# Kernel tuning notes

Measured on AMD Instinct MI355X. Metric: run time of the kernel, lower is better.

Reference implementation:

```python
import jax, jax.numpy as jnp
import numpy as np
import math

H = 128          # node_dim == hidden_dim
TED = 128        # time_emb_dim
T = 64
BN = 4096


def _mlp(x, w1, b1, w2, b2):
    # 2-layer MLP with SiLU, matching MLP(n_layer=2, act_fn=SiLU)
    return jax.nn.silu(x @ w1 + b1) @ w2 + b2


def _timestep_embedding(t, dim):
    # get_timestep_embedding for possibly-negative relative indices
    half = dim // 2
    freqs = jnp.exp(jnp.arange(half, dtype=jnp.float32) * (-math.log(10000.0) / (half - 1)))
    arg = t.astype(jnp.float32)[:, None] * freqs[None, :]
    return jnp.concatenate([jnp.sin(arg), jnp.cos(arg)], axis=-1)


def setup_inputs() -> dict:
    key = jax.random.key(0)
    ks = jax.random.split(key, 20)
    s = 1.0 / math.sqrt(H)
    d = {
        "x": jax.random.normal(ks[0], (BN, 3, T), jnp.float32),
        "h": jax.random.normal(ks[1], (BN, H, T), jnp.float32),
        "q_w1": jax.random.normal(ks[2], (H, H), jnp.float32) * s,
        "q_b1": jnp.zeros((H,), jnp.float32),
        "q_w2": jax.random.normal(ks[3], (H, H), jnp.float32) * s,
        "q_b2": jnp.zeros((H,), jnp.float32),
        "k_w1": jax.random.normal(ks[4], (H, H), jnp.float32) * s,
        "k_b1": jnp.zeros((H,), jnp.float32),
        "k_w2": jax.random.normal(ks[5], (H, H), jnp.float32) * s,
        "k_b2": jnp.zeros((H,), jnp.float32),
        "v_w1": jax.random.normal(ks[6], (H, H), jnp.float32) * s,
        "v_b1": jnp.zeros((H,), jnp.float32),
        "v_w2": jax.random.normal(ks[7], (H, H), jnp.float32) * s,
        "v_b2": jnp.zeros((H,), jnp.float32),
        "xm_w1": jax.random.normal(ks[8], (H, H), jnp.float32) * s,
        "xm_b1": jnp.zeros((H,), jnp.float32),
        "xm_w2": jax.random.normal(ks[9], (H, 1), jnp.float32) * s,
        "xm_b2": jnp.zeros((1,), jnp.float32),
        "t_w": jax.random.normal(ks[10], (TED, H), jnp.float32) * (1.0 / math.sqrt(TED)),
        "t_b": jnp.zeros((H,), jnp.float32),
    }
    return d


def reference(x, h, q_w1, q_b1, q_w2, q_b2, k_w1, k_b1, k_w2, k_b2,
              v_w1, v_b1, v_w2, v_b2, xm_w1, xm_b1, xm_w2, xm_b2, t_w, t_b):
    Tn = x.shape[-1]
    # relative time embedding E[t, s, :] of shape [T, T, H]
    ti = jnp.arange(Tn)
    rel = (ti[:, None] - ti[None, :]).reshape(-1)
    E = (_timestep_embedding(rel, TED) @ t_w + t_b).reshape(Tn, Tn, -1)

    # merge_time_dim: [N, H, T] -> [N*T, H]  (token order: node-major, time-minor)
    tok = h.transpose(0, 2, 1)                      # [N, T, H]
    q = _mlp(tok, q_w1, q_b1, q_w2, q_b2)           # [N, T, H]
    k = _mlp(tok, k_w1, k_b1, k_w2, k_b2)           # [N, T, H]
    v = _mlp(tok, v_w1, v_b1, v_w2, v_b2)           # [N, T, H]
    vx = _mlp(v, xm_w1, xm_b1, xm_w2, xm_b2)[..., 0]  # [N, T]

    # scores: q . (k_s + E_ts)  -- decomposed, avoids materializing k_ts [N,H,T,T]
    scores = jnp.einsum('nth,nsh->nts', q, k) + jnp.einsum('nth,tsh->nts', q, E)
    alpha = jax.nn.softmax(scores, axis=-1)          # [N, T, S]

    # h update: sum_s alpha * (v_s + E_ts)
    dh = jnp.einsum('nts,nsh->nth', alpha, v) + jnp.einsum('nts,tsh->nth', alpha, E)
    h_out = h + dh.transpose(0, 2, 1)                # [N, H, T]

    # x update: x_t += sum_s alpha[t,s] * vx[s] * (x_t - x_s)
    w = alpha * vx[:, None, :]                       # [N, T, S]
    x_out = x + x * jnp.sum(w, axis=-1)[:, None, :] - jnp.einsum('nts,nds->ndt', w, x)
    return (x_out, h_out)
```

## Files before the change

kernel.cpp:

```cpp
#include <hip/hip_runtime.h>
#include <hip/hip_bf16.h>
#include <math.h>

#define NN 4096

typedef __attribute__((ext_vector_type(8))) short s8v;
typedef __attribute__((ext_vector_type(4))) float f4v;
typedef __attribute__((ext_vector_type(4))) unsigned int u32x4;
typedef __attribute__((ext_vector_type(2))) unsigned int u32x2;
typedef unsigned short u16;

static __device__ __forceinline__ f4v MFMA16(s8v a, s8v b, f4v c) {
  return __builtin_amdgcn_mfma_f32_16x16x32_bf16(a, b, c, 0, 0, 0);
}
static __device__ __forceinline__ u16 f2bf(float f) {
  union { float f; unsigned int u; } v; v.f = f;
  unsigned int r = v.u + 0x7fffu + ((v.u >> 16) & 1u);
  return (u16)(r >> 16);
}
static __device__ __forceinline__ float bf2f(u16 u) {
  union { unsigned int u; float f; } v; v.u = ((unsigned int)u) << 16;
  return v.f;
}
static __device__ __forceinline__ unsigned int cvt2u(float lo, float hi) {
  __hip_bfloat162 h = __float22bfloat162_rn(make_float2(lo, hi));
  union { __hip_bfloat162 b; unsigned int u; } c; c.b = h; return c.u;
}
static __device__ __forceinline__ float silu(float v) {
  return v * __builtin_amdgcn_rcpf(1.0f + __expf(-v));
}

#define SW(row, byte)  ((row) * 256 + ((byte) ^ (((row) & 7) << 4)))

#define FA_OFF 0
#define FB_OFF 49152
#define FC_OFF 98304
#define FD_OFF 131072

__global__ void prep_kernel(const float* __restrict__ qw1, const float* __restrict__ kw1,
                            const float* __restrict__ vw1, const float* __restrict__ qw2,
                            const float* __restrict__ kw2, const float* __restrict__ vw2,
                            const float* __restrict__ xmw1,
                            const float* __restrict__ t_w, const float* __restrict__ t_b,
                            u16* __restrict__ wsb) {
  const int b = blockIdx.x, tid = threadIdx.x;
  const int kt = tid >> 6, l = tid & 63, lr = l & 15, lk = l >> 4;
  if (b < 56) {
    const float* W; int mt; u16* base;
    if (b < 24)      { base = wsb + FA_OFF; mt = b;      W = (b < 8) ? qw1 : (b < 16) ? kw1 : vw1; }
    else if (b < 48) { base = wsb + FB_OFF; mt = b - 24; W = (mt < 8) ? qw2 : (mt < 16) ? kw2 : vw2; }
    else             { base = wsb + FC_OFF; mt = b - 48; W = xmw1; }
    const int ch = (mt & 7) * 16;
    u16 o[8];
#pragma unroll
    for (int j = 0; j < 8; ++j) o[j] = f2bf(W[(kt * 32 + lk * 8 + j) * 128 + ch + lr]);
    u32x4 pk;
#pragma unroll
    for (int i = 0; i < 4; ++i) pk[i] = (unsigned int)o[2 * i] | ((unsigned int)o[2 * i + 1] << 16);
    *(u32x4*)&base[((mt * 4 + kt) * 64 + l) * 8] = pk;
  } else {
    const int rt = b - 56;
    const int r = rt * 16 + lr;
    const float rel = (float)(r - 63);
    const int h0 = kt * 32 + lk * 8;
    float acc[8];
#pragma unroll
    for (int j = 0; j < 8; ++j) acc[j] = t_b[h0 + j];
    const float C = -logf(10000.0f) / 63.0f;
    for (int i = 0; i < 64; ++i) {
      float f = expf((float)i * C);
      float a = rel * f;
      float sn = sinf(a), cs = cosf(a);
#pragma unroll
      for (int j = 0; j < 8; ++j) acc[j] = fmaf(sn, t_w[i * 128 + h0 + j], acc[j]);
#pragma unroll
      for (int j = 0; j < 8; ++j) acc[j] = fmaf(cs, t_w[(i + 64) * 128 + h0 + j], acc[j]);
    }
    u16 o[8];
#pragma unroll
    for (int j = 0; j < 8; ++j) o[j] = f2bf(acc[j]);
    u32x4 pk;
#pragma unroll
    for (int i = 0; i < 4; ++i) pk[i] = (unsigned int)o[2 * i] | ((unsigned int)o[2 * i + 1] << 16);
    *(u32x4*)&wsb[FC_OFF + (((8 + rt) * 4 + kt) * 64 + l) * 8] = pk;
    const int ct = h0 >> 4, lrp = h0 & 15;
    const int ktp = r >> 5, lkp = (r >> 3) & 3, jp = r & 7;
#pragma unroll
    for (int j = 0; j < 8; ++j)
      wsb[FD_OFF + ((ct * 4 + ktp) * 64 + lkp * 16 + lrp + j) * 8 + jp] = o[j];
  }
}

static __device__ __forceinline__ void ldfrag(s8v* dst, const u16* __restrict__ base,
                                              int tile, int l) {
#pragma unroll
  for (int kt = 0; kt < 4; ++kt) dst[kt] = *(const s8v*)&base[tile * 2048 + kt * 512 + l * 8];
}

template <bool SILU, bool HASB>
static __device__ __forceinline__ void gemm2(const s8v* f0, const s8v* f1,
                                             const unsigned char* Bl, unsigned char* Ol,
                                             const float* __restrict__ bias, int mt0,
                                             int lr, int lk, int swm, const int* rb) {
  f4v acc[2][4];
#pragma unroll
  for (int mi = 0; mi < 2; ++mi) {
    float bj[4];
#pragma unroll
    for (int j = 0; j < 4; ++j) bj[j] = HASB ? bias[(mt0 + mi) * 16 + lk * 4 + j] : 0.f;
#pragma unroll
    for (int ni = 0; ni < 4; ++ni)
#pragma unroll
      for (int j = 0; j < 4; ++j) acc[mi][ni][j] = bj[j];
  }
  __builtin_amdgcn_s_setprio(1);
#pragma unroll
  for (int kt = 0; kt < 4; ++kt) {
    s8v a0 = f0[kt], a1 = f1[kt];
#pragma unroll
    for (int ni = 0; ni < 4; ++ni) {
      s8v b = *(const s8v*)(Bl + ni * 4096 + rb[kt]);
      acc[0][ni] = MFMA16(a0, b, acc[0][ni]);
      acc[1][ni] = MFMA16(a1, b, acc[1][ni]);
    }
  }
  __builtin_amdgcn_s_setprio(0);
#pragma unroll
  for (int mi = 0; mi < 2; ++mi) {
    const int ob = lr * 256 + ((((mt0 + mi) * 32) + lk * 8) ^ swm);
#pragma unroll
    for (int ni = 0; ni < 4; ++ni) {
      float v0 = acc[mi][ni][0], v1 = acc[mi][ni][1], v2 = acc[mi][ni][2], v3 = acc[mi][ni][3];
      if (SILU) { v0 = silu(v0); v1 = silu(v1); v2 = silu(v2); v3 = silu(v3); }
      u32x2 st; st[0] = cvt2u(v0, v1); st[1] = cvt2u(v2, v3);
      *(u32x2*)(Ol + ni * 4096 + ob) = st;
    }
  }
}

__launch_bounds__(512, 4)
__global__ void et_main(const float* __restrict__ xg, const float* __restrict__ hg,
                        const u16* __restrict__ wsb,
                        const float* __restrict__ qb1, const float* __restrict__ qb2,
                        const float* __restrict__ kb1,
                        const float* __restrict__ vb1, const float* __restrict__ vb2,
                        const float* __restrict__ xmb1, const float* __restrict__ xmw2,
                        const float* __restrict__ xmb2,
                        float* __restrict__ xout, float* __restrict__ hout) {
  __shared__ __align__(16) unsigned char smem[81920];
  unsigned char* S0 = smem;
  unsigned char* S1 = smem + 16384;
  unsigned char* S2 = smem + 32768;
  unsigned char* S3 = smem + 49152;
  unsigned char* S4 = smem + 65536;
  unsigned char* ALP = S2;
  unsigned char* YB  = S2 + 8192;
  float* XLS = (float*)(S2 + 10240);
  float* VXP = (float*)(S2 + 11264);

  const u16* FA = wsb + FA_OFF;
  const u16* FB = wsb + FB_OFF;
  const u16* FC = wsb + FC_OFF;
  const u16* FD = wsb + FD_OFF;

  const int tid = threadIdx.x;
  const int l = tid & 63;
  const int lr = l & 15, lk = l >> 4;
  const int w = __builtin_amdgcn_readfirstlane(tid >> 6);
  const int u = w & 3;
  const bool lo = w < 4;
  const int ni0 = (w >> 2) * 2;
  const int mt0 = 2 * u;
  const int n = blockIdx.x;
  const size_t hbase = (size_t)n * 8192;
  const int swm = (lr & 7) << 4;
  int rb[4], hrb[2];
#pragma unroll
  for (int kt = 0; kt < 4; ++kt) rb[kt] = lr * 256 + ((kt * 64 + lk * 16) ^ swm);
#pragma unroll
  for (int kt = 0; kt < 2; ++kt) hrb[kt] = lr * 128 + ((kt * 64 + lk * 16) ^ swm);

  s8v fq[4], fk[4], fv[4];
  ldfrag(fq, FA, w, l); ldfrag(fk, FA, 8 + w, l); ldfrag(fv, FA, 16 + w, l);
  {
    int t = tid & 63, c0 = (tid >> 6) * 2;
#pragma unroll
    for (int cc = 0; cc < 2; ++cc) {
      int c = c0 + cc;
      float hv[8];
#pragma unroll
      for (int j = 0; j < 8; ++j) hv[j] = hg[hbase + (size_t)(c * 8 + j) * 64 + t];
      u32x4 pk;
#pragma unroll
      for (int j = 0; j < 4; ++j) pk[j] = cvt2u(hv[2 * j], hv[2 * j + 1]);
      *(u32x4*)(S0 + SW(t, c * 16)) = pk;
    }
  }
  __syncthreads();

  {
    f4v aq[4], ak[4], av[4];
#pragma unroll
    for (int ni = 0; ni < 4; ++ni)
#pragma unroll
      for (int j = 0; j < 4; ++j) {
        aq[ni][j] = qb1[w * 16 + lk * 4 + j];
        ak[ni][j] = kb1[w * 16 + lk * 4 + j];
        av[ni][j] = vb1[w * 16 + lk * 4 + j];
      }
    __builtin_amdgcn_s_setprio(1);
#pragma unroll
    for (int kt = 0; kt < 4; ++kt) {
      s8v a0 = fq[kt], a1 = fk[kt], a2 = fv[kt];
#pragma unroll
      for (int ni = 0; ni < 4; ++ni) {
        s8v b = *(const s8v*)(S0 + ni * 4096 + rb[kt]);
        aq[ni] = MFMA16(a0, b, aq[ni]);
        ak[ni] = MFMA16(a1, b, ak[ni]);
        av[ni] = MFMA16(a2, b, av[ni]);
      }
    }
    __builtin_amdgcn_s_setprio(0);
    const int ob = lr * 256 + ((w * 32 + lk * 8) ^ swm);
#pragma unroll
    for (int ni = 0; ni < 4; ++ni) {
      u32x2 s0v, s1v, s2v;
      s0v[0] = cvt2u(silu(aq[ni][0]), silu(aq[ni][1]));
      s0v[1] = cvt2u(silu(aq[ni][2]), silu(aq[ni][3]));
      s1v[0] = cvt2u(silu(ak[ni][0]), silu(ak[ni][1]));
      s1v[1] = cvt2u(silu(ak[ni][2]), silu(ak[ni][3]));
      s2v[0] = cvt2u(silu(av[ni][0]), silu(av[ni][1]));
      s2v[1] = cvt2u(silu(av[ni][2]), silu(av[ni][3]));
      *(u32x2*)(S1 + ni * 4096 + ob) = s0v;
      *(u32x2*)(S2 + ni * 4096 + ob) = s1v;
      *(u32x2*)(S3 + ni * 4096 + ob) = s2v;
    }
  }
  s8v fA0[4], fA1[4];
  if (lo) { ldfrag(fA0, FB, 2 * w, l);      ldfrag(fA1, FB, 2 * w + 1, l); }
  else    { ldfrag(fA0, FB, 16 + 2 * u, l); ldfrag(fA1, FB, 16 + 2 * u + 1, l); }
  __syncthreads();

  if (lo) gemm2<false, true>(fA0, fA1, S1, S4, qb2, 2 * w, lr, lk, swm, rb);
  else    gemm2<false, true>(fA0, fA1, S3, S0, vb2, 2 * u, lr, lk, swm, rb);
  if (lo) { ldfrag(fA0, FB, 8 + 2 * w, l); ldfrag(fA1, FB, 8 + 2 * w + 1, l); }
  else    { ldfrag(fA0, FC, 8 + 2 * u, l); ldfrag(fA1, FC, 8 + 2 * u + 1, l); }
  __syncthreads();

  if (lo) {
    gemm2<false, false>(fA0, fA1, S2, S1, nullptr, 2 * w, lr, lk, swm, rb);
  } else {
    f4v acc[2][4];
#pragma unroll
    for (int mi = 0; mi < 2; ++mi)
#pragma unroll
      for (int ni = 0; ni < 4; ++ni)
#pragma unroll
        for (int j = 0; j < 4; ++j) acc[mi][ni][j] = 0.f;
    __builtin_amdgcn_s_setprio(1);
#pragma unroll
    for (int kt = 0; kt < 4; ++kt) {
      s8v a0 = fA0[kt], a1 = fA1[kt];
#pragma unroll
      for (int ni = 0; ni < 4; ++ni) {
        s8v b = *(const s8v*)(S4 + ni * 4096 + rb[kt]);
        acc[0][ni] = MFMA16(a0, b, acc[0][ni]);
        acc[1][ni] = MFMA16(a1, b, acc[1][ni]);
      }
    }
    __builtin_amdgcn_s_setprio(0);
#pragma unroll
    for (int mi = 0; mi < 2; ++mi) {
      const int rbase = (2 * u + mi) * 16 + lk * 4;
#pragma unroll
      for (int ni = 0; ni < 4; ++ni) {
        int t = ni * 16 + lr;
        unsigned int p0 = cvt2u(acc[mi][ni][0], acc[mi][ni][1]);
        unsigned int p1 = cvt2u(acc[mi][ni][2], acc[mi][ni][3]);
        int i0 = rbase - t;
        if ((unsigned)(i0 + 0) < 64u) *(u16*)(S3 + t * 128 + ((2 * (i0 + 0)) ^ swm)) = (u16)(p0 & 0xffffu);
        if ((unsigned)(i0 + 1) < 64u) *(u16*)(S3 + t * 128 + ((2 * (i0 + 1)) ^ swm)) = (u16)(p0 >> 16);
        if ((unsigned)(i0 + 2) < 64u) *(u16*)(S3 + t * 128 + ((2 * (i0 + 2)) ^ swm)) = (u16)(p1 & 0xffffu);
        if ((unsigned)(i0 + 3) < 64u) *(u16*)(S3 + t * 128 + ((2 * (i0 + 3)) ^ swm)) = (u16)(p1 >> 16);
      }
    }
  }
  if (!lo) { ldfrag(fA0, FC, 2 * u, l); ldfrag(fA1, FC, 2 * u + 1, l); }
  __syncthreads();

  if (lo) {
    const int n0 = w * 16, t = n0 + lr;
    s8v bq[4];
#pragma unroll
    for (int kt = 0; kt < 4; ++kt) bq[kt] = *(const s8v*)(S4 + n0 * 256 + rb[kt]);
    f4v acc[4];
#pragma unroll
    for (int mi = 0; mi < 4; ++mi)
#pragma unroll
      for (int j = 0; j < 4; ++j) acc[mi][j] = 0.f;
    __builtin_amdgcn_s_setprio(1);
#pragma unroll
    for (int kt = 0; kt < 4; ++kt)
#pragma unroll
      for (int mi = 0; mi < 4; ++mi)
        acc[mi] = MFMA16(*(const s8v*)(S1 + mi * 4096 + rb[kt]), bq[kt], acc[mi]);
    __builtin_amdgcn_s_setprio(0);
    float e[4][4];
#pragma unroll
    for (int mi = 0; mi < 4; ++mi) {
      u32x2 qv = *(const u32x2*)(S3 + t * 128 + ((120 - 32 * mi - 8 * lk) ^ swm));
      e[mi][3] = acc[mi][3] + bf2f((u16)(qv[0] & 0xffffu));
      e[mi][2] = acc[mi][2] + bf2f((u16)(qv[0] >> 16));
      e[mi][1] = acc[mi][1] + bf2f((u16)(qv[1] & 0xffffu));
      e[mi][0] = acc[mi][0] + bf2f((u16)(qv[1] >> 16));
    }
    float m = e[0][0];
#pragma unroll
    for (int mi = 0; mi < 4; ++mi)
#pragma unroll
      for (int j = 0; j < 4; ++j) m = fmaxf(m, e[mi][j]);
    m = fmaxf(m, __shfl_xor(m, 16, 64));
    m = fmaxf(m, __shfl_xor(m, 32, 64));
    float s = 0.f;
#pragma unroll
    for (int mi = 0; mi < 4; ++mi)
#pragma unroll
      for (int j = 0; j < 4; ++j) { e[mi][j] = __expf(e[mi][j] - m); s += e[mi][j]; }
    s += __shfl_xor(s, 16, 64);
    s += __shfl_xor(s, 32, 64);
    float inv = __builtin_amdgcn_rcpf(s);
    unsigned int apk[8];
#pragma unroll
    for (int mi = 0; mi < 4; ++mi) {
      apk[2 * mi]     = cvt2u(e[mi][0] * inv, e[mi][1] * inv);
      apk[2 * mi + 1] = cvt2u(e[mi][2] * inv, e[mi][3] * inv);
      u32x2 st; st[0] = apk[2 * mi]; st[1] = apk[2 * mi + 1];
      *(u32x2*)(ALP + t * 128 + ((mi * 32 + lk * 8) ^ swm)) = st;
    }
    u32x4 zz; zz[0] = zz[1] = zz[2] = zz[3] = 0;
#pragma unroll
    for (int c = 0; c < 4; ++c) *(u32x4*)(S4 + t * 256 + lk * 64 + c * 16) = zz;
#pragma unroll
    for (int mi = 0; mi < 4; ++mi) {
      int rr = t + 63 - mi * 16 - lk * 4;
      *(u16*)(S4 + t * 256 + ((2 * (rr - 0)) ^ swm)) = (u16)(apk[2 * mi] & 0xffffu);
      *(u16*)(S4 + t * 256 + ((2 * (rr - 1)) ^ swm)) = (u16)(apk[2 * mi] >> 16);
      *(u16*)(S4 + t * 256 + ((2 * (rr - 2)) ^ swm)) = (u16)(apk[2 * mi + 1] & 0xffffu);
      *(u16*)(S4 + t * 256 + ((2 * (rr - 3)) ^ swm)) = (u16)(apk[2 * mi + 1] >> 16);
    }
  } else {
    f4v acc[2][4];
#pragma unroll
    for (int mi = 0; mi < 2; ++mi)
#pragma unroll
      for (int ni = 0; ni < 4; ++ni)
#pragma unroll
        for (int j = 0; j < 4; ++j) acc[mi][ni][j] = xmb1[(2 * u + mi) * 16 + lk * 4 + j];
    __builtin_amdgcn_s_setprio(1);
#pragma unroll
    for (int kt = 0; kt < 4; ++kt) {
      s8v a0 = fA0[kt], a1 = fA1[kt];
#pragma unroll
      for (int ni = 0; ni < 4; ++ni) {
        s8v b = *(const s8v*)(S0 + ni * 4096 + rb[kt]);
        acc[0][ni] = MFMA16(a0, b, acc[0][ni]);
        acc[1][ni] = MFMA16(a1, b, acc[1][ni]);
      }
    }
    __builtin_amdgcn_s_setprio(0);
#pragma unroll
    for (int mi = 0; mi < 2; ++mi) {
      float w2[4];
#pragma unroll
      for (int j = 0; j < 4; ++j) w2[j] = xmw2[(2 * u + mi) * 16 + lk * 4 + j];
#pragma unroll
      for (int ni = 0; ni < 4; ++ni) {
        float s = 0.f;
#pragma unroll
        for (int j = 0; j < 4; ++j) s = fmaf(silu(acc[mi][ni][j]), w2[j], s);
        s += __shfl_xor(s, 16, 64);
        s += __shfl_xor(s, 32, 64);
        if (l < 16) VXP[(2 * u + mi) * 64 + ni * 16 + l] = s;
      }
    }
  }
  s8v fd0[4], fd1[4];
  ldfrag(fd0, FD, mt0, l); ldfrag(fd1, FD, mt0 + 1, l);
  __syncthreads();

  float hld[16];
#pragma unroll
  for (int mi = 0; mi < 2; ++mi)
#pragma unroll
    for (int nj = 0; nj < 2; ++nj) {
      size_t base = hbase + (size_t)((mt0 + mi) * 16 + lk * 4) * 64 + (ni0 + nj) * 16 + lr;
#pragma unroll
      for (int j = 0; j < 4; ++j) hld[(mi * 2 + nj) * 4 + j] = hg[base + j * 64];
    }
  if (!lo) {
    const int t0 = (u & 1) * 32;
    const int c = ((u >> 1) << 6) + l;
    unsigned int pk[16];
#pragma unroll
    for (int i2 = 0; i2 < 16; ++i2) {
      int t = t0 + 2 * i2;
      u16 v0 = *(const u16*)(S0 + t * 256 + ((2 * c) ^ ((t & 7) << 4)));
      u16 v1 = *(const u16*)(S0 + (t + 1) * 256 + ((2 * c) ^ (((t + 1) & 7) << 4)));
      pk[i2] = (unsigned int)v0 | ((unsigned int)v1 << 16);
    }
    const int cm = (c & 7) << 4;
#pragma unroll
    for (int cc = 0; cc < 4; ++cc) {
      u32x4 st; st[0] = pk[4 * cc]; st[1] = pk[4 * cc + 1]; st[2] = pk[4 * cc + 2]; st[3] = pk[4 * cc + 3];
      *(u32x4*)(S3 + c * 128 + ((t0 * 2 + cc * 16) ^ cm)) = st;
    }
  } else if (w == 0) {
    int t = l;
    float vx = xmb2[0];
#pragma unroll
    for (int pt = 0; pt < 8; ++pt) vx += VXP[pt * 64 + t];
    float x0 = xg[n * 192 + t], x1 = xg[n * 192 + 64 + t], x2 = xg[n * 192 + 128 + t];
    XLS[t] = x0; XLS[64 + t] = x1; XLS[128 + t] = x2;
    unsigned int p0 = cvt2u(vx, vx * x0), p1 = cvt2u(vx * x1, vx * x2);
    *(u16*)(YB + 0   + ((2 * t) ^ 0))  = (u16)(p0 & 0xffffu);
    *(u16*)(YB + 128 + ((2 * t) ^ 16)) = (u16)(p0 >> 16);
    *(u16*)(YB + 256 + ((2 * t) ^ 32)) = (u16)(p1 & 0xffffu);
    *(u16*)(YB + 384 + ((2 * t) ^ 48)) = (u16)(p1 >> 16);
  } else if (w == 1) {
    u32x4 zz; zz[0] = zz[1] = zz[2] = zz[3] = 0;
    *(u32x4*)(YB + 512 + l * 16) = zz;
  } else if (w == 2) {
    if (l < 32) { u32x4 zz; zz[0] = zz[1] = zz[2] = zz[3] = 0; *(u32x4*)(YB + 1536 + l * 16) = zz; }
  }
  __syncthreads();

  {
    f4v acc[2][2];
#pragma unroll
    for (int mi = 0; mi < 2; ++mi)
#pragma unroll
      for (int nj = 0; nj < 2; ++nj)
#pragma unroll
        for (int j = 0; j < 4; ++j) acc[mi][nj][j] = 0.f;
    __builtin_amdgcn_s_setprio(1);
#pragma unroll
    for (int kt = 0; kt < 2; ++kt) {
      s8v a0 = *(const s8v*)(S3 + (mt0)     * 2048 + hrb[kt]);
      s8v a1 = *(const s8v*)(S3 + (mt0 + 1) * 2048 + hrb[kt]);
#pragma unroll
      for (int nj = 0; nj < 2; ++nj) {
        s8v b = *(const s8v*)(ALP + (ni0 + nj) * 2048 + hrb[kt]);
        acc[0][nj] = MFMA16(a0, b, acc[0][nj]);
        acc[1][nj] = MFMA16(a1, b, acc[1][nj]);
      }
    }
#pragma unroll
    for (int kt = 0; kt < 4; ++kt) {
      s8v a0 = fd0[kt], a1 = fd1[kt];
#pragma unroll
      for (int nj = 0; nj < 2; ++nj) {
        s8v b = *(const s8v*)(S4 + (ni0 + nj) * 4096 + rb[kt]);
        acc[0][nj] = MFMA16(a0, b, acc[0][nj]);
        acc[1][nj] = MFMA16(a1, b, acc[1][nj]);
      }
    }
    __builtin_amdgcn_s_setprio(0);
#pragma unroll
    for (int mi = 0; mi < 2; ++mi)
#pragma unroll
      for (int nj = 0; nj < 2; ++nj) {
        size_t base = hbase + (size_t)((mt0 + mi) * 16 + lk * 4) * 64 + (ni0 + nj) * 16 + lr;
#pragma unroll
        for (int j = 0; j < 4; ++j)
          hout[base + j * 64] = hld[(mi * 2 + nj) * 4 + j] + acc[mi][nj][j];
      }
    if (lo) {
      f4v xa;
#pragma unroll
      for (int j = 0; j < 4; ++j) xa[j] = 0.f;
#pragma unroll
      for (int kt = 0; kt < 2; ++kt)
        xa = MFMA16(*(const s8v*)(YB + hrb[kt]),
                    *(const s8v*)(ALP + w * 2048 + hrb[kt]), xa);
      if (lk == 0) {
        int t = w * 16 + lr;
        float a1 = xa[0];
#pragma unroll
        for (int d = 0; d < 3; ++d) {
          float xv = XLS[d * 64 + t];
          xout[n * 192 + d * 64 + t] = fmaf(xv, a1, xv) - xa[1 + d];
        }
      }
    }
  }
}

extern "C" void kernel_launch(void* const* d_in, const int* in_sizes, int n_in,
                              void* d_out, int out_size, void* d_ws, size_t ws_size,
                              hipStream_t stream) {
  const float* xg   = (const float*)d_in[0];
  const float* hg   = (const float*)d_in[1];
  const float* qw1  = (const float*)d_in[2];
  const float* qb1  = (const float*)d_in[3];
  const float* qw2  = (const float*)d_in[4];
  const float* qb2  = (const float*)d_in[5];
  const float* kw1  = (const float*)d_in[6];
  const float* kb1  = (const float*)d_in[7];
  const float* kw2  = (const float*)d_in[8];
  const float* vw1  = (const float*)d_in[10];
  const float* vb1  = (const float*)d_in[11];
  const float* vw2  = (const float*)d_in[12];
  const float* vb2  = (const float*)d_in[13];
  const float* xmw1 = (const float*)d_in[14];
  const float* xmb1 = (const float*)d_in[15];
  const float* xmw2 = (const float*)d_in[16];
  const float* xmb2 = (const float*)d_in[17];
  const float* t_w  = (const float*)d_in[18];
  const float* t_b  = (const float*)d_in[19];

  u16* wsb = (u16*)d_ws;
  float* xout = (float*)d_out;
  float* hout = xout + (size_t)NN * 192;

  prep_kernel<<<64, 256, 0, stream>>>(qw1, kw1, vw1, qw2, kw2, vw2, xmw1, t_w, t_b, wsb);
  et_main<<<NN, 512, 0, stream>>>(xg, hg, wsb,
                                  qb1, qb2, kb1, vb1, vb2, xmb1, xmw2, xmb2,
                                  xout, hout);
}
```

Before: 170.3 us.

## Transpose final dh GEMM so h loads and stores use float4 along time

Reorganizes the final h-update MFMA so each wave owns one time tile and four channel tiles, swapping operand roles so accumulator rows map to time. This lets the residual h loads and h_out stores use contiguous float4 accesses along the time dimension instead of scalar strided ones. The FD weight fragments are now partly prefetched before the barrier and partly loaded from global inside the loop. Bias and weight loads are also vectorized to float4, and the softmax max becomes a tree reduction. The main risk is extra global loads of weight fragments inside the MFMA loop and higher register use.

```diff
diff --git a/kernel.cpp b/kernel.cpp
--- a/kernel.cpp
+++ b/kernel.cpp
@@ -105,13 +105,13 @@
   f4v acc[2][4];
 #pragma unroll
   for (int mi = 0; mi < 2; ++mi) {
-    float bj[4];
-#pragma unroll
-    for (int j = 0; j < 4; ++j) bj[j] = HASB ? bias[(mt0 + mi) * 16 + lk * 4 + j] : 0.f;
-#pragma unroll
-    for (int ni = 0; ni < 4; ++ni)
-#pragma unroll
-      for (int j = 0; j < 4; ++j) acc[mi][ni][j] = bj[j];
+    float4 b4 = make_float4(0.f, 0.f, 0.f, 0.f);
+    if (HASB) b4 = *(const float4*)&bias[(mt0 + mi) * 16 + lk * 4];
+#pragma unroll
+    for (int ni = 0; ni < 4; ++ni) {
+      acc[mi][ni][0] = b4.x; acc[mi][ni][1] = b4.y;
+      acc[mi][ni][2] = b4.z; acc[mi][ni][3] = b4.w;
+    }
   }
   __builtin_amdgcn_s_setprio(1);
 #pragma unroll
@@ -169,8 +169,8 @@
   const int w = __builtin_amdgcn_readfirstlane(tid >> 6);
   const int u = w & 3;
   const bool lo = w < 4;
-  const int ni0 = (w >> 2) * 2;
-  const int mt0 = 2 * u;
+  const int mt = u;
+  const int ct0 = (w >> 2) * 4;
   const int n = blockIdx.x;
   const size_t hbase = (size_t)n * 8192;
   const int swm = (lr & 7) << 4;
@@ -199,15 +199,16 @@
   __syncthreads();
 
   {
+    const float4 bq = *(const float4*)&qb1[w * 16 + lk * 4];
+    const float4 bk = *(const float4*)&kb1[w * 16 + lk * 4];
+    const float4 bv = *(const float4*)&vb1[w * 16 + lk * 4];
     f4v aq[4], ak[4], av[4];
 #pragma unroll
-    for (int ni = 0; ni < 4; ++ni)
-#pragma unroll
-      for (int j = 0; j < 4; ++j) {
-        aq[ni][j] = qb1[w * 16 + lk * 4 + j];
-        ak[ni][j] = kb1[w * 16 + lk * 4 + j];
-        av[ni][j] = vb1[w * 16 + lk * 4 + j];
-      }
+    for (int ni = 0; ni < 4; ++ni) {
+      aq[ni][0] = bq.x; aq[ni][1] = bq.y; aq[ni][2] = bq.z; aq[ni][3] = bq.w;
+      ak[ni][0] = bk.x; ak[ni][1] = bk.y; ak[ni][2] = bk.z; ak[ni][3] = bk.w;
+      av[ni][0] = bv.x; av[ni][1] = bv.y; av[ni][2] = bv.z; av[ni][3] = bv.w;
+    }
     __builtin_amdgcn_s_setprio(1);
 #pragma unroll
     for (int kt = 0; kt < 4; ++kt) {
@@ -314,11 +315,11 @@
       e[mi][1] = acc[mi][1] + bf2f((u16)(qv[1] & 0xffffu));
       e[mi][0] = acc[mi][0] + bf2f((u16)(qv[1] >> 16));
     }
-    float m = e[0][0];
-#pragma unroll
-    for (int mi = 0; mi < 4; ++mi)
-#pragma unroll
-      for (int j = 0; j < 4; ++j) m = fmaxf(m, e[mi][j]);
+    float m01 = fmaxf(fmaxf(e[0][0], e[0][1]), fmaxf(e[0][2], e[0][3]));
+    float m11 = fmaxf(fmaxf(e[1][0], e[1][1]), fmaxf(e[1][2], e[1][3]));
+    float m21 = fmaxf(fmaxf(e[2][0], e[2][1]), fmaxf(e[2][2], e[2][3]));
+    float m31 = fmaxf(fmaxf(e[3][0], e[3][1]), fmaxf(e[3][2], e[3][3]));
+    float m = fmaxf(fmaxf(m01, m11), fmaxf(m21, m31));
     m = fmaxf(m, __shfl_xor(m, 16, 64));
     m = fmaxf(m, __shfl_xor(m, 32, 64));
     float s = 0.f;
@@ -349,13 +350,14 @@
       *(u16*)(S4 + t * 256 + ((2 * (rr - 3)) ^ swm)) = (u16)(apk[2 * mi + 1] >> 16);
     }
   } else {
+    const float4 bx0 = *(const float4*)&xmb1[(2 * u) * 16 + lk * 4];
+    const float4 bx1 = *(const float4*)&xmb1[(2 * u + 1) * 16 + lk * 4];
     f4v acc[2][4];
 #pragma unroll
-    for (int mi = 0; mi < 2; ++mi)
-#pragma unroll
-      for (int ni = 0; ni < 4; ++ni)
-#pragma unroll
-        for (int j = 0; j < 4; ++j) acc[mi][ni][j] = xmb1[(2 * u + mi) * 16 + lk * 4 + j];
+    for (int ni = 0; ni < 4; ++ni) {
+      acc[0][ni][0] = bx0.x; acc[0][ni][1] = bx0.y; acc[0][ni][2] = bx0.z; acc[0][ni][3] = bx0.w;
+      acc[1][ni][0] = bx1.x; acc[1][ni][1] = bx1.y; acc[1][ni][2] = bx1.z; acc[1][ni][3] = bx1.w;
+    }
     __builtin_amdgcn_s_setprio(1);
 #pragma unroll
     for (int kt = 0; kt < 4; ++kt) {
@@ -370,33 +372,21 @@
     __builtin_amdgcn_s_setprio(0);
 #pragma unroll
     for (int mi = 0; mi < 2; ++mi) {
-      float w2[4];
-#pragma unroll
-      for (int j = 0; j < 4; ++j) w2[j] = xmw2[(2 * u + mi) * 16 + lk * 4 + j];
+      const float4 w4 = *(const float4*)&xmw2[(2 * u + mi) * 16 + lk * 4];
 #pragma unroll
       for (int ni = 0; ni < 4; ++ni) {
-        float s = 0.f;
-#pragma unroll
-        for (int j = 0; j < 4; ++j) s = fmaf(silu(acc[mi][ni][j]), w2[j], s);
+        float s = silu(acc[mi][ni][0]) * w4.x;
+        s = fmaf(silu(acc[mi][ni][1]), w4.y, s);
+        s = fmaf(silu(acc[mi][ni][2]), w4.z, s);
+        s = fmaf(silu(acc[mi][ni][3]), w4.w, s);
         s += __shfl_xor(s, 16, 64);
         s += __shfl_xor(s, 32, 64);
         if (l < 16) VXP[(2 * u + mi) * 64 + ni * 16 + l] = s;
       }
     }
   }
-  s8v fd0[4], fd1[4];
-  ldfrag(fd0, FD, mt0, l); ldfrag(fd1, FD, mt0 + 1, l);
   __syncthreads();
 
-  float hld[16];
-#pragma unroll
-  for (int mi = 0; mi < 2; ++mi)
-#pragma unroll
-    for (int nj = 0; nj < 2; ++nj) {
-      size_t base = hbase + (size_t)((mt0 + mi) * 16 + lk * 4) * 64 + (ni0 + nj) * 16 + lr;
-#pragma unroll
-      for (int j = 0; j < 4; ++j) hld[(mi * 2 + nj) * 4 + j] = hg[base + j * 64];
-    }
   if (!lo) {
     const int t0 = (u & 1) * 32;
     const int c = ((u >> 1) << 6) + l;
@@ -432,48 +422,54 @@
   } else if (w == 2) {
     if (l < 32) { u32x4 zz; zz[0] = zz[1] = zz[2] = zz[3] = 0; *(u32x4*)(YB + 1536 + l * 16) = zz; }
   }
+  float4 hld[4];
+#pragma unroll
+  for (int nt = 0; nt < 4; ++nt)
+    hld[nt] = *(const float4*)&hg[hbase + (size_t)((ct0 + nt) * 16 + lr) * 64 + mt * 16 + lk * 4];
+  s8v fpre[8];
+#pragma unroll
+  for (int nt = 0; nt < 2; ++nt)
+#pragma unroll
+    for (int kt = 0; kt < 4; ++kt)
+      fpre[nt * 4 + kt] = *(const s8v*)&FD[((ct0 + nt) * 4 + kt) * 512 + l * 8];
   __syncthreads();
 
   {
-    f4v acc[2][2];
-#pragma unroll
-    for (int mi = 0; mi < 2; ++mi)
-#pragma unroll
-      for (int nj = 0; nj < 2; ++nj)
-#pragma unroll
-        for (int j = 0; j < 4; ++j) acc[mi][nj][j] = 0.f;
+    s8v aA0 = *(const s8v*)(ALP + mt * 2048 + hrb[0]);
+    s8v aA1 = *(const s8v*)(ALP + mt * 2048 + hrb[1]);
+    s8v aB[4];
+#pragma unroll
+    for (int kt = 0; kt < 4; ++kt) aB[kt] = *(const s8v*)(S4 + mt * 4096 + rb[kt]);
+    f4v acc[4];
+#pragma unroll
+    for (int nt = 0; nt < 4; ++nt)
+#pragma unroll
+      for (int j = 0; j < 4; ++j) acc[nt][j] = 0.f;
     __builtin_amdgcn_s_setprio(1);
 #pragma unroll
-    for (int kt = 0; kt < 2; ++kt) {
-      s8v a0 = *(const s8v*)(S3 + (mt0)     * 2048 + hrb[kt]);
-      s8v a1 = *(const s8v*)(S3 + (mt0 + 1) * 2048 + hrb[kt]);
-#pragma unroll
-      for (int nj = 0; nj < 2; ++nj) {
-        s8v b = *(const s8v*)(ALP + (ni0 + nj) * 2048 + hrb[kt]);
-        acc[0][nj] = MFMA16(a0, b, acc[0][nj]);
-        acc[1][nj] = MFMA16(a1, b, acc[1][nj]);
-      }
-    }
-#pragma unroll
-    for (int kt = 0; kt < 4; ++kt) {
-      s8v a0 = fd0[kt], a1 = fd1[kt];
-#pragma unroll
-      for (int nj = 0; nj < 2; ++nj) {
-        s8v b = *(const s8v*)(S4 + (ni0 + nj) * 4096 + rb[kt]);
-        acc[0][nj] = MFMA16(a0, b, acc[0][nj]);
-        acc[1][nj] = MFMA16(a1, b, acc[1][nj]);
+    for (int nt = 0; nt < 4; ++nt) {
+      s8v bv0 = *(const s8v*)(S3 + (ct0 + nt) * 2048 + hrb[0]);
+      s8v bv1 = *(const s8v*)(S3 + (ct0 + nt) * 2048 + hrb[1]);
+      acc[nt] = MFMA16(aA0, bv0, acc[nt]);
+      acc[nt] = MFMA16(aA1, bv1, acc[nt]);
+#pragma unroll
+      for (int kt = 0; kt < 4; ++kt) {
+        s8v bf = (nt < 2) ? fpre[nt * 4 + kt]
+                          : *(const s8v*)&FD[((ct0 + nt) * 4 + kt) * 512 + l * 8];
+        acc[nt] = MFMA16(aB[kt], bf, acc[nt]);
       }
     }
     __builtin_amdgcn_s_setprio(0);
 #pragma unroll
-    for (int mi = 0; mi < 2; ++mi)
-#pragma unroll
-      for (int nj = 0; nj < 2; ++nj) {
-        size_t base = hbase + (size_t)((mt0 + mi) * 16 + lk * 4) * 64 + (ni0 + nj) * 16 + lr;
-#pragma unroll
-        for (int j = 0; j < 4; ++j)
-          hout[base + j * 64] = hld[(mi * 2 + nj) * 4 + j] + acc[mi][nj][j];
-      }
+    for (int nt = 0; nt < 4; ++nt) {
+      size_t off = hbase + (size_t)((ct0 + nt) * 16 + lr) * 64 + mt * 16 + lk * 4;
+      float4 o;
+      o.x = hld[nt].x + acc[nt][0];
+      o.y = hld[nt].y + acc[nt][1];
+      o.z = hld[nt].z + acc[nt][2];
+      o.w = hld[nt].w + acc[nt][3];
+      *(float4*)&hout[off] = o;
+    }
     if (lo) {
       f4v xa;
 #pragma unroll
```

Result: slower. 187.3 us (+10.0%).
